# Kernel optimization log

Measured on AMD Instinct MI355X. Metric: run time of the kernel, lower is better.

The kernel has to match this reference:

```python
import jax, jax.numpy as jnp
from jax import lax
import numpy as np

B, H, W = 1, 128, 256
C = 32           # feature_channels
D = 32           # max_disp
HID = 64         # hidden_channels in message passing
ITERS = 5


def conv2d(x, w, b):
    # x: [N, Cin, H, W], w: [Cout, Cin, kh, kw], SAME padding, stride 1
    y = lax.conv_general_dilated(x, w, (1, 1), [(1, 1), (1, 1)],
                                 dimension_numbers=('NCHW', 'OIHW', 'NCHW'))
    return y + b[None, :, None, None]


def setup_inputs() -> dict:
    key = jax.random.key(0)
    ks = jax.random.split(key, 12)
    def p(k, shape, s=0.05):
        return jax.random.normal(k, shape, jnp.float32) * s
    return {
        'left_img':  jax.random.normal(ks[0], (B, 3, H, W), jnp.float32),
        'right_img': jax.random.normal(ks[1], (B, 3, H, W), jnp.float32),
        # feature extractor (3 -> C -> C)
        'fe_w1': p(ks[2], (C, 3, 3, 3)),  'fe_b1': jnp.zeros((C,), jnp.float32),
        'fe_w2': p(ks[3], (C, C, 3, 3)),  'fe_b2': jnp.zeros((C,), jnp.float32),
        # cost volume 1x1 conv over concat(left, shifted_right): 2C -> 1
        'cv_w': p(ks[4], (2 * C,)),       'cv_b': jnp.zeros((), jnp.float32),
        # message passing: concat(feature, belief)=C+1 -> HID -> 1
        'mp_w1': p(ks[5], (HID, C + 1, 3, 3)), 'mp_b1': jnp.zeros((HID,), jnp.float32),
        'mp_w2': p(ks[6], (1, HID, 3, 3)),     'mp_b2': jnp.zeros((1,), jnp.float32),
        # refinement: concat(left_img, disparity)=4 -> 32 -> 32 -> 1 residual
        'rf_w1': p(ks[7], (32, 4, 3, 3)),  'rf_b1': jnp.zeros((32,), jnp.float32),
        'rf_w2': p(ks[8], (32, 32, 3, 3)), 'rf_b2': jnp.zeros((32,), jnp.float32),
        'rf_w3': p(ks[9], (1, 32, 3, 3)),  'rf_b3': jnp.zeros((1,), jnp.float32),
    }


def _forward(left_img, right_img, fe_w1, fe_b1, fe_w2, fe_b2, cv_w, cv_b,
             mp_w1, mp_b1, mp_w2, mp_b2, rf_w1, rf_b1, rf_w2, rf_b2, rf_w3, rf_b3):
    def feat(img):
        h = jax.nn.relu(conv2d(img, fe_w1, fe_b1))
        return jax.nn.relu(conv2d(h, fe_w2, fe_b2))

    lf = feat(left_img)    # [B, C, H, W]
    rf = feat(right_img)   # [B, C, H, W]

    # Cost volume: shift right features by each disparity, 1x1 conv on concat.
    rf_sh = jnp.stack([jnp.pad(rf, ((0, 0), (0, 0), (0, 0), (d, 0)))[..., :W]
                       for d in range(D)])                     # [D, B, C, H, W]
    pair = jnp.concatenate([jnp.broadcast_to(lf[None], rf_sh.shape), rf_sh], axis=2)  # [D,B,2C,H,W]
    cost = jnp.einsum('dbchw,c->dbhw', pair, cv_w) + cv_b      # [D, B, H, W]
    data = cost[:, :, None]                                     # [D, B, 1, H, W]

    # Iterative BP message passing, vectorized across all disparity planes.
    def mp(data_term):  # data_term: [B, 1, H, W]
        def step(belief, _):
            x = jnp.concatenate([lf, belief], axis=1)           # [B, C+1, H, W]
            hdn = jax.nn.relu(conv2d(x, mp_w1, mp_b1))          # [B, HID, H, W]
            msg = conv2d(hdn, mp_w2, mp_b2)                     # [B, 1, H, W]
            return data_term + msg, None
        belief, _ = lax.scan(step, data_term, None, length=ITERS)
        return belief

    beliefs = jax.vmap(mp)(data)                                # [D, B, 1, H, W]
    refined = jnp.transpose(beliefs, (1, 2, 0, 3, 4))           # [B, 1, D, H, W]

    prob = jax.nn.softmax(-refined, axis=2)                     # [B, 1, D, H, W]
    idx = jnp.arange(D, dtype=prob.dtype)
    disparity = jnp.einsum('bodhw,d->bohw', prob, idx)          # [B, 1, H, W]

    # Refinement network (residual).
    x = jnp.concatenate([left_img, disparity], axis=1)          # [B, 4, H, W]
    r = jax.nn.relu(conv2d(x, rf_w1, rf_b1))
    r = jax.nn.relu(conv2d(r, rf_w2, rf_b2))
    res = conv2d(r, rf_w3, rf_b3)
    return disparity + res                                      # [B, 1, H, W]


def reference(left_img, right_img, fe_w1, fe_b1, fe_w2, fe_b2, cv_w, cv_b,
              mp_w1, mp_b1, mp_w2, mp_b2, rf_w1, rf_b1, rf_w2, rf_b2, rf_w3, rf_b3):
    return _forward(left_img, right_img, fe_w1, fe_b1, fe_w2, fe_b2, cv_w, cv_b,
                    mp_w1, mp_b1, mp_w2, mp_b2, rf_w1, rf_b1, rf_w2, rf_b2, rf_w3, rf_b3)
```

## Files before the change

kernel.cpp:

```cpp
#include <hip/hip_runtime.h>
#include <hip/hip_bf16.h>

#define H 128
#define W 256
#define HW (H*W)
#define NC 32
#define ND 32
#define NHID 64

template<int NCO>
__global__ __launch_bounds__(256) void conv3x3(
        const float* __restrict__ in0, const float* __restrict__ in1,
        float* __restrict__ out0, float* __restrict__ out1,
        const float* __restrict__ w, const float* __restrict__ b,
        int CIN, int COUT, int wstride, int dorelu,
        const float* __restrict__ addin, int tpose) {
    __shared__ float tile[2][4][10][35];
    const int tid = threadIdx.x;
    const int zg = (COUT + NCO - 1) / NCO;
    const int img = blockIdx.z / zg;
    const int cog = blockIdx.z % zg;
    const float* in = img ? in1 : in0;
    float* out = img ? out1 : out0;
    const int cobase = cog * NCO;
    int nco = COUT - cobase; if (nco > NCO) nco = NCO;
    const int gx0 = blockIdx.x * 32, gy0 = blockIdx.y * 8;
    const int tx = tid & 31, ty = tid >> 5;

    const int nst = (CIN + 3) >> 2;
    {
        int nch = CIN < 4 ? CIN : 4;
        for (int i = tid; i < nch * 340; i += 256) {
            int ch = i / 340, rem = i % 340;
            int r = rem / 34, cc = rem % 34;
            int gy = gy0 + r - 1, gx = gx0 + cc - 1;
            tile[0][ch][r][cc] = (gy >= 0 && gy < H && gx >= 0 && gx < W)
                                 ? in[(size_t)ch * HW + gy * W + gx] : 0.f;
        }
    }
    __syncthreads();

    float acc[NCO];
#pragma unroll
    for (int i = 0; i < NCO; i++) acc[i] = 0.f;

    for (int s = 0; s < nst; s++) {
        const int c0 = s * 4;
        int nch = CIN - c0; if (nch > 4) nch = 4;
        if (s + 1 < nst) {
            const int c1 = c0 + 4;
            int nch2 = CIN - c1; if (nch2 > 4) nch2 = 4;
            const int nb = (s + 1) & 1;
            for (int i = tid; i < nch2 * 340; i += 256) {
                int ch = i / 340, rem = i % 340;
                int r = rem / 34, cc = rem % 34;
                int gy = gy0 + r - 1, gx = gx0 + cc - 1;
                tile[nb][ch][r][cc] = (gy >= 0 && gy < H && gx >= 0 && gx < W)
                                      ? in[(size_t)(c1 + ch) * HW + gy * W + gx] : 0.f;
            }
        }
        const int cb = s & 1;
        for (int ch = 0; ch < nch; ch++) {
            float v[9];
#pragma unroll
            for (int ky = 0; ky < 3; ky++)
#pragma unroll
                for (int kx = 0; kx < 3; kx++)
                    v[ky * 3 + kx] = tile[cb][ch][ty + ky][tx + kx];
            const float* wrow = w + (size_t)cobase * wstride + (size_t)(c0 + ch) * 9;
#pragma unroll
            for (int co = 0; co < NCO; co++) {
                if (co < nco) {
                    const float* wp = wrow + (size_t)co * wstride;
#pragma unroll
                    for (int k = 0; k < 9; k++) acc[co] += wp[k] * v[k];
                }
            }
        }
        __syncthreads();
    }

    const int gy = gy0 + ty, gx = gx0 + tx;
    const float ad = addin ? addin[gy * W + gx] : 0.f;
    if (tpose) {
        float* op = out + (size_t)(gy * W + gx) * 64 + cobase;
#pragma unroll
        for (int co = 0; co < NCO; co++) {
            if (co < nco) {
                float r = acc[co] + b[cobase + co];
                if (dorelu) r = fmaxf(r, 0.f);
                op[co] = r + ad;
            }
        }
    } else {
#pragma unroll
        for (int co = 0; co < NCO; co++) {
            if (co < nco) {
                float r = acc[co] + b[cobase + co];
                if (dorelu) r = fmaxf(r, 0.f);
                r += ad;
                out[(size_t)(cobase + co) * HW + gy * W + gx] = r;
            }
        }
    }
}

__global__ __launch_bounds__(256) void aconv(
        const float* __restrict__ lf, float* __restrict__ At,
        const float* __restrict__ w, const float* __restrict__ b) {
    const int tid = threadIdx.x;
    const int lane = tid & 63;
    const int lw = __builtin_amdgcn_readfirstlane(tid >> 6);
    const int wid = blockIdx.x * 4 + lw;
    const int y = wid >> 5;
    const int x0 = (wid & 31) * 8;
    const bool xL = (x0 == 0), xR = (x0 == W - 8);

    const float* wl = w + lane * 297;
    float acc[8];
#pragma unroll
    for (int i = 0; i < 8; i++) acc[i] = 0.f;

#pragma unroll 2
    for (int cin = 0; cin < 32; ++cin) {
        float iv[3][10];
#pragma unroll
        for (int r = 0; r < 3; r++) {
            int yy = y - 1 + r;
            if (yy < 0 || yy >= H) {
#pragma unroll
                for (int q = 0; q < 10; q++) iv[r][q] = 0.f;
            } else {
                const float* rp = lf + (size_t)cin * HW + yy * W;
                if (xL) {
                    iv[r][0] = 0.f;
#pragma unroll
                    for (int q = 1; q < 10; q++) iv[r][q] = rp[q - 1];
                } else if (xR) {
#pragma unroll
                    for (int q = 0; q < 9; q++) iv[r][q] = rp[x0 - 1 + q];
                    iv[r][9] = 0.f;
                } else {
#pragma unroll
                    for (int q = 0; q < 10; q++) iv[r][q] = rp[x0 - 1 + q];
                }
            }
        }
        float wv[9];
#pragma unroll
        for (int k = 0; k < 9; k++) wv[k] = wl[cin * 9 + k];
#pragma unroll
        for (int ky = 0; ky < 3; ky++)
#pragma unroll
            for (int kx = 0; kx < 3; kx++)
#pragma unroll
                for (int i = 0; i < 8; i++)
                    acc[i] += wv[ky * 3 + kx] * iv[ky][i + kx];
    }

    const float bb = b[lane];
    float* op = At + (size_t)(y * W + x0) * 64 + lane;
#pragma unroll
    for (int i = 0; i < 8; i++) op[i * 64] = acc[i] + bb;
}

__global__ void chan_cost(const float* __restrict__ lf, const float* __restrict__ rf,
                          const float* __restrict__ cvw, const float* __restrict__ cvb,
                          float* __restrict__ cost, float* __restrict__ bel) {
    __shared__ float rsS[W];
    const int x = threadIdx.x;
    const int p = blockIdx.x * W + x;
    float ls = 0.f, rs = 0.f;
    for (int c = 0; c < NC; c++) {
        ls += lf[c * HW + p] * cvw[c];
        rs += rf[c * HW + p] * cvw[NC + c];
    }
    rsS[x] = rs;
    ls += cvb[0];
    __syncthreads();
#pragma unroll
    for (int d = 0; d < ND; d++) {
        float cc = ls + (x >= d ? rsS[x - d] : 0.f);
        cost[(size_t)d * HW + p] = cc;
        bel[(size_t)d * HW + p] = cc;
    }
}

#define LOADROW(YC, AR)                                                        \
  {                                                                            \
    if ((YC) >= 0 && (YC) < H) {                                               \
      AR[0] = bp[e0off];                                                       \
      _Pragma("unroll") for (int j = 1; j < 17; j++) AR[j] = bp[(j - 8) * 64]; \
      AR[17] = bp[e17off];                                                     \
    }                                                                          \
    bp += W * 64;                                                              \
  }

#define LOADBEL(Z, BR)                                                         \
  {                                                                            \
    const int z_ = (Z);                                                        \
    if (z_ >= 0 && z_ < H) {                                                   \
      const float* br_ = beld + (size_t)z_ * W + x0;                           \
      BR[0] = xnot0 ? br_[-2] : 0.f;                                           \
      BR[1] = xnot0 ? br_[-1] : 0.f;                                           \
      _Pragma("unroll") for (int q = 0; q < 16; q++) BR[q + 2] = br_[q];       \
      BR[18] = xnotE ? br_[16] : 0.f;                                          \
      BR[19] = xnotE ? br_[17] : 0.f;                                          \
    } else {                                                                   \
      _Pragma("unroll") for (int q = 0; q < 20; q++) BR[q] = 0.f;              \
    }                                                                          \
  }

#define COMPUTE(U, AR, HARR, B0, B1, B2)                                       \
  {                                                                            \
    const int yc_ = y0 + (U);                                                  \
    if (yc_ < 0 || yc_ >= H) {                                                 \
      _Pragma("unroll") for (int j = 0; j < 18; j++) HARR[j] = 0.f;            \
    } else {                                                                   \
      _Pragma("unroll") for (int j = 0; j < 18; j++) {                         \
        float acc_ = AR[j];                                                    \
        acc_ += w1[0] * B0[j] + w1[1] * B0[j + 1] + w1[2] * B0[j + 2];         \
        acc_ += w1[3] * B1[j] + w1[4] * B1[j + 1] + w1[5] * B1[j + 2];         \
        acc_ += w1[6] * B2[j] + w1[7] * B2[j + 1] + w1[8] * B2[j + 2];         \
        HARR[j] = fmaxf(acc_, 0.f);                                            \
      }                                                                        \
      if (x0 == 0) HARR[0] = 0.f;                                              \
      if (x0 == W - 16) HARR[17] = 0.f;                                        \
    }                                                                          \
  }

#define EMIT3(T, HH2, HH1, HH0)                                                \
  {                                                                            \
    _Pragma("unroll") for (int jo = 0; jo < 16; jo++) {                        \
      float pp = w2[0] * HH2[jo] + w2[1] * HH2[jo + 1] + w2[2] * HH2[jo + 2]   \
               + w2[3] * HH1[jo] + w2[4] * HH1[jo + 1] + w2[5] * HH1[jo + 2]   \
               + w2[6] * HH0[jo] + w2[7] * HH0[jo + 1] + w2[8] * HH0[jo + 2];  \
      partW[jo][lane] = pp;                                                    \
    }                                                                          \
    {                                                                          \
      const float4* pr = (const float4*)&partW[pq][qq * 16];                   \
      float cg_ = cost[obase + (size_t)(T) * W];                               \
      float4 v0 = pr[0], v1 = pr[1];                                           \
      float s_ = ((v0.x + v0.y) + (v0.z + v0.w)) +                             \
                 ((v1.x + v1.y) + (v1.z + v1.w));                              \
      float4 v2 = pr[2], v3 = pr[3];                                           \
      s_ += ((v2.x + v2.y) + (v2.z + v2.w)) +                                  \
            ((v3.x + v3.y) + (v3.z + v3.w));                                   \
      s_ += __shfl_xor(s_, 16);                                                \
      s_ += __shfl_xor(s_, 32);                                                \
      if (qq == 0) bout[obase + (size_t)(T) * W] = cg_ + s_ + b2;              \
    }                                                                          \
  }

#define STEP(T, AIN, AOUT, HX2, HX1, HX0, B0, B1, B2, BN, DOLOAD, DOBEL)       \
  {                                                                            \
    if (DOBEL) { LOADBEL(y0 + (T) + 3, BN); }                                  \
    if (DOLOAD) { LOADROW(y0 + (T) + 2, AOUT); }                               \
    COMPUTE((T) + 1, AIN, HX0, B0, B1, B2);                                    \
    EMIT3(T, HX2, HX1, HX0);                                                   \
  }

__global__ __launch_bounds__(256, 4) void mp_iter_fast(
    const float* __restrict__ At,
    const float* __restrict__ cost,
    const float* __restrict__ bin,
    float* __restrict__ bout,
    const float* __restrict__ mp_w1,
    const float* __restrict__ mp_w2,
    const float* __restrict__ mp_b2) {
    __shared__ float partS[4][16][68];

    const int tid = threadIdx.x;
    const int lane = tid & 63;
    const int lw = __builtin_amdgcn_readfirstlane(tid >> 6);
    float (*partW)[68] = partS[lw];

    const int i = blockIdx.x;
    const int xcd = i & 7;
    const int jj = i >> 3;
    const int ybl = jj & 1;
    const int sl = (jj >> 1) & 15;
    const int d4 = jj >> 5;
    const int d = d4 * 4 + lw;
    const int x0 = sl * 16;
    const int y0 = (xcd + 8 * ybl) * 8;
    const bool xnot0 = (x0 > 0), xnotE = (x0 < W - 16);

    float w1[9], w2[9];
#pragma unroll
    for (int k = 0; k < 9; k++) {
        w1[k] = mp_w1[lane * 297 + 288 + k];
        w2[k] = mp_w2[lane * 9 + k];
    }
    const float b2 = mp_b2[0];

    const float* bp = At + (size_t)(y0 - 1) * (W * 64) + (x0 + 7) * 64 + lane;
    const int e0off  = (x0 == 0)      ? -448 : -512;
    const int e17off = (x0 == W - 16) ?  512 :  576;

    const float* beld = bin + (size_t)d * HW;
    const int pq = lane & 15, qq = lane >> 4;
    const size_t obase = (size_t)d * HW + (size_t)y0 * W + x0 + pq;

    float aA[18], aB[18];
    float hA[18], hB[18], hC[18];
    float bl0[20], bl1[20], bl2[20], bl3[20];

    LOADBEL(y0 - 2, bl0);
    LOADBEL(y0 - 1, bl1);
    LOADBEL(y0,     bl2);
    LOADROW(y0 - 1, aA);
    LOADROW(y0,     aB);
    COMPUTE(-1, aA, hA, bl0, bl1, bl2);
    LOADBEL(y0 + 1, bl3);
    LOADROW(y0 + 1, aA);
    COMPUTE(0, aB, hB, bl1, bl2, bl3);
    LOADBEL(y0 + 2, bl0);

    STEP(0, aA, aB, hA, hB, hC, bl2, bl3, bl0, bl1, 1, 1)
    STEP(1, aB, aA, hB, hC, hA, bl3, bl0, bl1, bl2, 1, 1)
    STEP(2, aA, aB, hC, hA, hB, bl0, bl1, bl2, bl3, 1, 1)
    STEP(3, aB, aA, hA, hB, hC, bl1, bl2, bl3, bl0, 1, 1)
    STEP(4, aA, aB, hB, hC, hA, bl2, bl3, bl0, bl1, 1, 1)
    STEP(5, aB, aA, hC, hA, hB, bl3, bl0, bl1, bl2, 1, 1)
    STEP(6, aA, aB, hA, hB, hC, bl0, bl1, bl2, bl3, 1, 1)
    STEP(7, aB, aA, hB, hC, hA, bl1, bl2, bl3, bl0, 0, 0)
}

__global__ void softmax_disp(const float* __restrict__ bel, const float* __restrict__ left,
                             float* __restrict__ disp, float* __restrict__ x4) {
    int p = blockIdx.x * 256 + threadIdx.x;
    if (p >= HW) return;
    float v[ND];
    float m = -1e30f;
#pragma unroll
    for (int d = 0; d < ND; d++) {
        v[d] = -bel[d * HW + p];
        m = fmaxf(m, v[d]);
    }
    float s = 0.f, ws = 0.f;
#pragma unroll
    for (int d = 0; d < ND; d++) {
        float e = __expf(v[d] - m);
        s += e;
        ws += e * (float)d;
    }
    float dv = ws / s;
    disp[p] = dv;
    x4[3 * HW + p] = dv;
    x4[p] = left[p];
    x4[HW + p] = left[HW + p];
    x4[2 * HW + p] = left[2 * HW + p];
}

extern "C" void kernel_launch(void* const* d_in, const int* in_sizes, int n_in,
                              void* d_out, int out_size, void* d_ws, size_t ws_size,
                              hipStream_t stream) {
    const float* left   = (const float*)d_in[0];
    const float* right  = (const float*)d_in[1];
    const float* fe_w1  = (const float*)d_in[2];
    const float* fe_b1  = (const float*)d_in[3];
    const float* fe_w2  = (const float*)d_in[4];
    const float* fe_b2  = (const float*)d_in[5];
    const float* cv_w   = (const float*)d_in[6];
    const float* cv_b   = (const float*)d_in[7];
    const float* mp_w1  = (const float*)d_in[8];
    const float* mp_b1  = (const float*)d_in[9];
    const float* mp_w2  = (const float*)d_in[10];
    const float* mp_b2  = (const float*)d_in[11];
    const float* rf_w1  = (const float*)d_in[12];
    const float* rf_b1  = (const float*)d_in[13];
    const float* rf_w2  = (const float*)d_in[14];
    const float* rf_b2  = (const float*)d_in[15];
    const float* rf_w3  = (const float*)d_in[16];
    const float* rf_b3  = (const float*)d_in[17];
    float* out = (float*)d_out;

    float* ws = (float*)d_ws;
    float* At    = ws;
    float* tmp0  = ws;
    float* tmp1  = ws + 1048576;
    float* lf    = ws + 2097152;
    float* rfeat = ws + 3145728;
    float* cost  = ws + 4194304;
    float* bel   = ws + 5242880;
    float* bel2  = ws + 6291456;
    float* disp  = ws + 7405568;
    float* x4    = ws + 7438336;

    dim3 blk(256);

    conv3x3<4><<<dim3(8, 16, 16), blk, 0, stream>>>(left, right, tmp0, tmp1, fe_w1, fe_b1, 3, 32, 27, 1, nullptr, 0);
    conv3x3<4><<<dim3(8, 16, 16), blk, 0, stream>>>(tmp0, tmp1, lf, rfeat, fe_w2, fe_b2, 32, 32, 288, 1, nullptr, 0);

    aconv<<<dim3(1024), blk, 0, stream>>>(lf, At, mp_w1, mp_b1);

    chan_cost<<<dim3(H), blk, 0, stream>>>(lf, rfeat, cv_w, cv_b, cost, bel);

    dim3 gmp(2048);
    mp_iter_fast<<<gmp, blk, 0, stream>>>(At, cost, bel,  bel2, mp_w1, mp_w2, mp_b2);
    mp_iter_fast<<<gmp, blk, 0, stream>>>(At, cost, bel2, bel,  mp_w1, mp_w2, mp_b2);
    mp_iter_fast<<<gmp, blk, 0, stream>>>(At, cost, bel,  bel2, mp_w1, mp_w2, mp_b2);
    mp_iter_fast<<<gmp, blk, 0, stream>>>(At, cost, bel2, bel,  mp_w1, mp_w2, mp_b2);
    mp_iter_fast<<<gmp, blk, 0, stream>>>(At, cost, bel,  bel2, mp_w1, mp_w2, mp_b2);

    softmax_disp<<<dim3(HW / 256), blk, 0, stream>>>(bel2, left, disp, x4);

    conv3x3<4><<<dim3(8, 16, 8), blk, 0, stream>>>(x4, x4, At, At, rf_w1, rf_b1, 4, 32, 36, 1, nullptr, 0);
    conv3x3<4><<<dim3(8, 16, 8), blk, 0, stream>>>(At, At, rfeat, rfeat, rf_w2, rf_b2, 32, 32, 288, 1, nullptr, 0);
    conv3x3<4><<<dim3(8, 16, 1), blk, 0, stream>>>(rfeat, rfeat, out, out, rf_w3, rf_b3, 32, 1, 288, 0, disp, 0);
}
```

Measured before the change: 453.4 us.

## Replace tiled 3x3 convs with lane-per-output-channel direct conv kernels

Result: slower. 490.1 us (+8.1%).

```diff
diff --git a/kernel.cpp b/kernel.cpp
--- a/kernel.cpp
+++ b/kernel.cpp
@@ -102,6 +102,117 @@
                 out[(size_t)(cobase + co) * HW + gy * W + gx] = r;
             }
         }
+    }
+}
+
+template<int CIN>
+__global__ __launch_bounds__(256) void dconv(
+        const float* __restrict__ in0, const float* __restrict__ in1,
+        float* __restrict__ out0, float* __restrict__ out1,
+        const float* __restrict__ w, int wstride, const float* __restrict__ b) {
+    const int tid = threadIdx.x;
+    const int lane = tid & 63;
+    const int lw = __builtin_amdgcn_readfirstlane(tid >> 6);
+    const int wid = blockIdx.x * 4 + lw;
+    const int y = wid >> 5;
+    const int x0 = (wid & 31) * 8;
+    const bool xL = (x0 == 0), xR = (x0 == W - 8);
+    const int cout = lane & 31;
+    const float* in = (lane >> 5) ? in1 : in0;
+    float* out = (lane >> 5) ? out1 : out0;
+    const float* wl = w + (size_t)cout * wstride;
+
+    float acc[8];
+#pragma unroll
+    for (int i = 0; i < 8; i++) acc[i] = 0.f;
+
+#pragma unroll 2
+    for (int cin = 0; cin < CIN; ++cin) {
+        float wv[9];
+#pragma unroll
+        for (int k = 0; k < 9; k++) wv[k] = wl[cin * 9 + k];
+#pragma unroll
+        for (int r = 0; r < 3; r++) {
+            int yy = y - 1 + r;
+            if (yy < 0 || yy >= H) continue;
+            const float* rp = in + (size_t)cin * HW + yy * W + x0;
+            float riv[10];
+            riv[0] = xL ? 0.f : rp[-1];
+#pragma unroll
+            for (int q = 0; q < 8; q++) riv[q + 1] = rp[q];
+            riv[9] = xR ? 0.f : rp[8];
+#pragma unroll
+            for (int kx = 0; kx < 3; kx++)
+#pragma unroll
+                for (int i = 0; i < 8; i++)
+                    acc[i] += wv[r * 3 + kx] * riv[i + kx];
+        }
+    }
+    const float bb = b[cout];
+    float* op = out + (size_t)cout * HW + y * W + x0;
+    float4 o0, o1;
+    o0.x = fmaxf(acc[0] + bb, 0.f); o0.y = fmaxf(acc[1] + bb, 0.f);
+    o0.z = fmaxf(acc[2] + bb, 0.f); o0.w = fmaxf(acc[3] + bb, 0.f);
+    o1.x = fmaxf(acc[4] + bb, 0.f); o1.y = fmaxf(acc[5] + bb, 0.f);
+    o1.z = fmaxf(acc[6] + bb, 0.f); o1.w = fmaxf(acc[7] + bb, 0.f);
+    *(float4*)op = o0;
+    *(float4*)(op + 4) = o1;
+}
+
+template<int CIN>
+__global__ __launch_bounds__(256) void hconv(
+        const float* __restrict__ in, float* __restrict__ out,
+        const float* __restrict__ w, int wstride, const float* __restrict__ b) {
+    const int tid = threadIdx.x;
+    const int lane = tid & 63;
+    const int lw = __builtin_amdgcn_readfirstlane(tid >> 6);
+    const int wid = blockIdx.x * 4 + lw;
+    const int y = wid >> 5;
+    const int x0 = (wid & 31) * 8;
+    const bool xL = (x0 == 0), xR = (x0 == W - 8);
+    const int cout = lane & 31;
+    const int ch = lane >> 5;
+    const float* wl = w + (size_t)cout * wstride;
+
+    float acc[8];
+#pragma unroll
+    for (int i = 0; i < 8; i++) acc[i] = 0.f;
+
+#pragma unroll 2
+    for (int cb = 0; cb < CIN; cb += 2) {
+        const int cin = cb + ch;
+        float wv[9];
+#pragma unroll
+        for (int k = 0; k < 9; k++) wv[k] = wl[cin * 9 + k];
+#pragma unroll
+        for (int r = 0; r < 3; r++) {
+            int yy = y - 1 + r;
+            if (yy < 0 || yy >= H) continue;
+            const float* rp = in + (size_t)cin * HW + yy * W + x0;
+            float riv[10];
+            riv[0] = xL ? 0.f : rp[-1];
+#pragma unroll
+            for (int q = 0; q < 8; q++) riv[q + 1] = rp[q];
+            riv[9] = xR ? 0.f : rp[8];
+#pragma unroll
+            for (int kx = 0; kx < 3; kx++)
+#pragma unroll
+                for (int i = 0; i < 8; i++)
+                    acc[i] += wv[r * 3 + kx] * riv[i + kx];
+        }
+    }
+#pragma unroll
+    for (int i = 0; i < 8; i++) acc[i] += __shfl_xor(acc[i], 32);
+    if (ch == 0) {
+        const float bb = b[cout];
+        float* op = out + (size_t)cout * HW + y * W + x0;
+        float4 o0, o1;
+        o0.x = fmaxf(acc[0] + bb, 0.f); o0.y = fmaxf(acc[1] + bb, 0.f);
+        o0.z = fmaxf(acc[2] + bb, 0.f); o0.w = fmaxf(acc[3] + bb, 0.f);
+        o1.x = fmaxf(acc[4] + bb, 0.f); o1.y = fmaxf(acc[5] + bb, 0.f);
+        o1.z = fmaxf(acc[6] + bb, 0.f); o1.w = fmaxf(acc[7] + bb, 0.f);
+        *(float4*)op = o0;
+        *(float4*)(op + 4) = o1;
     }
 }
 
@@ -387,11 +498,12 @@
     float* bel2  = ws + 6291456;
     float* disp  = ws + 7405568;
     float* x4    = ws + 7438336;
+    float* r1    = ws + 7569408;
 
     dim3 blk(256);
 
-    conv3x3<4><<<dim3(8, 16, 16), blk, 0, stream>>>(left, right, tmp0, tmp1, fe_w1, fe_b1, 3, 32, 27, 1, nullptr, 0);
-    conv3x3<4><<<dim3(8, 16, 16), blk, 0, stream>>>(tmp0, tmp1, lf, rfeat, fe_w2, fe_b2, 32, 32, 288, 1, nullptr, 0);
+    dconv<3><<<dim3(1024), blk, 0, stream>>>(left, right, tmp0, tmp1, fe_w1, 27, fe_b1);
+    dconv<32><<<dim3(1024), blk, 0, stream>>>(tmp0, tmp1, lf, rfeat, fe_w2, 288, fe_b2);
 
     aconv<<<dim3(1024), blk, 0, stream>>>(lf, At, mp_w1, mp_b1);
 
@@ -406,7 +518,7 @@
 
     softmax_disp<<<dim3(HW / 256), blk, 0, stream>>>(bel2, left, disp, x4);
 
-    conv3x3<4><<<dim3(8, 16, 8), blk, 0, stream>>>(x4, x4, At, At, rf_w1, rf_b1, 4, 32, 36, 1, nullptr, 0);
-    conv3x3<4><<<dim3(8, 16, 8), blk, 0, stream>>>(At, At, rfeat, rfeat, rf_w2, rf_b2, 32, 32, 288, 1, nullptr, 0);
+    hconv<4><<<dim3(1024), blk, 0, stream>>>(x4, r1, rf_w1, 36, rf_b1);
+    hconv<32><<<dim3(1024), blk, 0, stream>>>(r1, rfeat, rf_w2, 288, rf_b2);
     conv3x3<4><<<dim3(8, 16, 1), blk, 0, stream>>>(rfeat, rfeat, out, out, rf_w3, rf_b3, 32, 1, 288, 0, disp, 0);
 }
```

## Replace shared-memory tiled conv with wave-per-row-segment register conv for 32-out convs

Applied to the files above, without the earlier changes.

Measured after the change: 658.9 us. 1.45x slower.

```diff
diff --git a/kernel.cpp b/kernel.cpp
--- a/kernel.cpp
+++ b/kernel.cpp
@@ -103,6 +103,64 @@
             }
         }
     }
+}
+
+template<int CIN>
+__global__ __launch_bounds__(256) void sconv(
+        const float* __restrict__ in0, const float* __restrict__ in1,
+        float* __restrict__ out0, float* __restrict__ out1,
+        const float* __restrict__ w, int wstride, const float* __restrict__ b) {
+    const int tid = threadIdx.x;
+    const int lane = tid & 63;
+    const int cout = lane & 31;
+    const int ph = lane >> 5;
+    const int lw = __builtin_amdgcn_readfirstlane(tid >> 6);
+    const int wid = blockIdx.x * 4 + lw;
+    const int y = wid >> 4;
+    const int xs = (wid & 15) * 16;
+    const bool xL = (xs == 0), xR = (xs == W - 16);
+    const float* in = blockIdx.y ? in1 : in0;
+    float* out = blockIdx.y ? out1 : out0;
+    const float* wl = w + (size_t)cout * wstride;
+
+    float acc[8];
+#pragma unroll
+    for (int i = 0; i < 8; i++) acc[i] = 0.f;
+
+#pragma unroll 2
+    for (int cin = 0; cin < CIN; ++cin) {
+        float wv[9];
+#pragma unroll
+        for (int k = 0; k < 9; k++) wv[k] = wl[cin * 9 + k];
+#pragma unroll
+        for (int r = 0; r < 3; r++) {
+            int yy = y - 1 + r;
+            if (yy < 0 || yy >= H) continue;
+            const float* rp = in + (size_t)cin * HW + yy * W + xs;
+            float w18[18];
+            w18[0] = xL ? 0.f : rp[-1];
+#pragma unroll
+            for (int j = 1; j < 17; j++) w18[j] = rp[j - 1];
+            w18[17] = xR ? 0.f : rp[16];
+            float riv[10];
+#pragma unroll
+            for (int j = 0; j < 10; j++) riv[j] = ph ? w18[j + 8] : w18[j];
+#pragma unroll
+            for (int kx = 0; kx < 3; kx++)
+#pragma unroll
+                for (int i = 0; i < 8; i++)
+                    acc[i] += wv[r * 3 + kx] * riv[i + kx];
+        }
+    }
+    const float bb = b[cout];
+    float* op = out + (size_t)cout * HW + y * W + xs + ph * 8;
+    float4 o0, o1;
+    o0.x = fmaxf(acc[0] + bb, 0.f); o0.y = fmaxf(acc[1] + bb, 0.f);
+    o0.z = fmaxf(acc[2] + bb, 0.f); o0.w = fmaxf(acc[3] + bb, 0.f);
+    o1.x = fmaxf(acc[4] + bb, 0.f); o1.y = fmaxf(acc[5] + bb, 0.f);
+    o1.z = fmaxf(acc[6] + bb, 0.f); o1.w = fmaxf(acc[7] + bb, 0.f);
+    *(float4*)op = o0;
+    *(float4*)(op + 4) = o1;
 }
 
 __global__ __launch_bounds__(256) void aconv(
@@ -387,11 +445,12 @@
     float* bel2  = ws + 6291456;
     float* disp  = ws + 7405568;
     float* x4    = ws + 7438336;
+    float* r1    = ws + 7569408;
 
     dim3 blk(256);
 
-    conv3x3<4><<<dim3(8, 16, 16), blk, 0, stream>>>(left, right, tmp0, tmp1, fe_w1, fe_b1, 3, 32, 27, 1, nullptr, 0);
-    conv3x3<4><<<dim3(8, 16, 16), blk, 0, stream>>>(tmp0, tmp1, lf, rfeat, fe_w2, fe_b2, 32, 32, 288, 1, nullptr, 0);
+    sconv<3><<<dim3(512, 2), blk, 0, stream>>>(left, right, tmp0, tmp1, fe_w1, 27, fe_b1);
+    sconv<32><<<dim3(512, 2), blk, 0, stream>>>(tmp0, tmp1, lf, rfeat, fe_w2, 288, fe_b2);
 
     aconv<<<dim3(1024), blk, 0, stream>>>(lf, At, mp_w1, mp_b1);
 
@@ -406,7 +465,7 @@
 
     softmax_disp<<<dim3(HW / 256), blk, 0, stream>>>(bel2, left, disp, x4);
 
-    conv3x3<4><<<dim3(8, 16, 8), blk, 0, stream>>>(x4, x4, At, At, rf_w1, rf_b1, 4, 32, 36, 1, nullptr, 0);
-    conv3x3<4><<<dim3(8, 16, 8), blk, 0, stream>>>(At, At, rfeat, rfeat, rf_w2, rf_b2, 32, 32, 288, 1, nullptr, 0);
+    sconv<4><<<dim3(512, 1), blk, 0, stream>>>(x4, x4, r1, r1, rf_w1, 36, rf_b1);
+    sconv<32><<<dim3(512, 1), blk, 0, stream>>>(r1, r1, rfeat, rfeat, rf_w2, 288, rf_b2);
     conv3x3<4><<<dim3(8, 16, 1), blk, 0, stream>>>(rfeat, rfeat, out, out, rf_w3, rf_b3, 32, 1, 288, 0, disp, 0);
 }
```
